# Kernel tuning notes

Measured on AMD Instinct MI355X. Metric: run time of the kernel, lower is better.

Reference implementation:

```python
import jax, jax.numpy as jnp
import numpy as np

B, T, S, A, H = 256, 256, 64, 16, 512  # batch, time, state_dim, action_dim, hypernet hidden


def setup_inputs() -> dict:
    key = jax.random.key(0)
    ks = jax.random.split(key, 12)
    x0 = jax.random.normal(ks[0], (B, S), dtype=jnp.float32)
    us = jax.random.normal(ks[1], (B, T, A), dtype=jnp.float32)
    # a_net: state_dim -> H -> S*S   (hypernetwork generating A(zx))
    Wa1 = jax.random.normal(ks[2], (S, H), dtype=jnp.float32) * 0.05
    ba1 = jax.random.normal(ks[3], (H,), dtype=jnp.float32) * 0.01
    Wa2 = jax.random.normal(ks[4], (H, S * S), dtype=jnp.float32) * 0.002  # small -> stable recurrence
    ba2 = jax.random.normal(ks[5], (S * S,), dtype=jnp.float32) * 0.002
    # b_net: action_dim -> H -> S*A  (hypernetwork generating B(zu))
    Wb1 = jax.random.normal(ks[6], (A, H), dtype=jnp.float32) * 0.05
    bb1 = jax.random.normal(ks[7], (H,), dtype=jnp.float32) * 0.01
    Wb2 = jax.random.normal(ks[8], (H, S * A), dtype=jnp.float32) * 0.02
    bb2 = jax.random.normal(ks[9], (S * A,), dtype=jnp.float32) * 0.02
    return {"x0": x0, "us": us, "Wa1": Wa1, "ba1": ba1, "Wa2": Wa2, "ba2": ba2,
            "Wb1": Wb1, "bb1": bb1, "Wb2": Wb2, "bb2": bb2}


def reference(x0, us, Wa1, ba1, Wa2, ba2, Wb1, bb1, Wb2, bb2):
    """HyperLinearSSM.rollout: x_{t+1} = A(x_t) @ x_t + B(u_t) @ u_t (zx=x, zu=u)."""
    def step(x, u):
        # hypernetwork-generated state matrix A(zx=x): [B, S, S]
        ha = jnp.tanh(x @ Wa1 + ba1)
        Amat = (ha @ Wa2 + ba2).reshape(-1, S, S)
        # hypernetwork-generated input matrix B(zu=u): [B, S, A]
        hb = jnp.tanh(u @ Wb1 + bb1)
        Bmat = (hb @ Wb2 + bb2).reshape(-1, S, A)
        x_next = jnp.einsum('bij,bj->bi', Amat, x) + jnp.einsum('bij,bj->bi', Bmat, u)
        return x_next, x_next

    us_t = jnp.transpose(us, (1, 0, 2))  # [T, B, A]
    _, xs = jax.lax.scan(step, x0, us_t)  # xs: [T, B, S]
    return jnp.transpose(xs, (1, 0, 2))   # [B, T, S]
```

## Files before the change

kernel.cpp:

```cpp
#include <hip/hip_runtime.h>

#define BSZ 256
#define TSZ 256
#define SSZ 64
#define ASZ 16
#define HSZ 512

typedef float f32x4 __attribute__((ext_vector_type(4)));
typedef short bf16x8 __attribute__((ext_vector_type(8)));
typedef unsigned short u16x8 __attribute__((ext_vector_type(8)));
typedef unsigned long long u64;
typedef unsigned short ushort_t;

#define XBUF_BYTES ((size_t)4 * BSZ * SSZ * sizeof(u64))
#define WT_ELEMS   ((size_t)4096 * 512)
#define WA1_ELEMS  ((size_t)64 * 512)
#define WS_NEEDED  (XBUF_BYTES + 3 * WT_ELEMS * sizeof(ushort_t) \
                    + 3 * WA1_ELEMS * sizeof(ushort_t))


#define XSTR        68
#define MF_X_OFF    0
#define MF_RED_OFF  4608
#define MF_HAH_OFF  5120
#define MF_HAM_OFF  (5120 + 18944)
#define MF_HAL_OFF  (24064 + 18944)
#define MF_WCH_OFF  (43008 + 18944)
#define MF_SMEM     (61952 + 2 * 49152)

#define NCH 16
#define HA_STR 20
#define X_OFF   0
#define HA_OFF  1024
#define W_OFF   (HA_OFF + HSZ * HA_STR)
#define RED_OFF (W_OFF + 3 * 32 * 256)
#define SMEM_FLOATS (RED_OFF + 512)
#define SMEM_BYTES  (SMEM_FLOATS * 4)

__device__ __forceinline__ void stage16(const void* gp, void* lp) {
    __builtin_amdgcn_global_load_lds(
        (const __attribute__((address_space(1))) void*)gp,
        (__attribute__((address_space(3))) void*)lp, 16, 0, 0);
}

__device__ __forceinline__ float wait_tag(const u64* p, unsigned tag) {
    u64 v = __hip_atomic_load(p, __ATOMIC_RELAXED, __HIP_MEMORY_SCOPE_AGENT);
    while ((unsigned)(v >> 32) != tag) {
        __builtin_amdgcn_s_sleep(1);
        v = __hip_atomic_load(p, __ATOMIC_RELAXED, __HIP_MEMORY_SCOPE_AGENT);
    }
    return __uint_as_float((unsigned)v);
}

__device__ __forceinline__ ushort_t f32_to_bf16(float f) {
    unsigned u = __float_as_uint(f);
    unsigned r = u + 0x7FFFu + ((u >> 16) & 1u);
    return (ushort_t)(r >> 16);
}
__device__ __forceinline__ float bf16_to_f32(ushort_t h) {
    return __uint_as_float((unsigned)h << 16);
}

__global__ __launch_bounds__(256) void wsplit_kernel(
    const float* __restrict__ Wa2,
    ushort_t* __restrict__ wth, ushort_t* __restrict__ wtm,
    ushort_t* __restrict__ wtl)
{
    __shared__ float tile[64][65];
    const int bc = blockIdx.x & 63;
    const int bh = blockIdx.x >> 6;
    const int c0 = bc * 64, h0 = bh * 64;
    const int tid = threadIdx.x;

    const int lr = tid >> 4, lc4 = (tid & 15) * 4;
    #pragma unroll
    for (int p = 0; p < 4; ++p) {
        const int h = p * 16 + lr;
        *(f32x4*)&tile[h][lc4] =
            *(const f32x4*)(Wa2 + (size_t)(h0 + h) * 4096 + c0 + lc4);
    }
    __syncthreads();

    const int col = tid >> 2, hb = (tid & 3) * 16;
    u16x8 H0, H1, M0, M1, L0, L1;
    #pragma unroll
    for (int q = 0; q < 16; ++q) {
        const float v = tile[hb + q][col];
        const ushort_t H = f32_to_bf16(v);
        const float r1 = v - bf16_to_f32(H);
        const ushort_t M = f32_to_bf16(r1);
        const ushort_t L = f32_to_bf16(r1 - bf16_to_f32(M));
        if (q < 8) { H0[q] = H; M0[q] = M; L0[q] = L; }
        else       { H1[q-8] = H; M1[q-8] = M; L1[q-8] = L; }
    }
    const int col_g = c0 + col;
    const int hbase = h0 + hb;
    const int kk    = hbase >> 5;
    const int sl0   = (hbase >> 3) & 3;
    const size_t atom0 = (((size_t)(col_g >> 5) * 16 + kk) * 4 + sl0) * 32
                       + (col_g & 31);
    const size_t atom1 = atom0 + 32;
    *(u16x8*)(wth + atom0 * 8) = H0;  *(u16x8*)(wth + atom1 * 8) = H1;
    *(u16x8*)(wtm + atom0 * 8) = M0;  *(u16x8*)(wtm + atom1 * 8) = M1;
    *(u16x8*)(wtl + atom0 * 8) = L0;  *(u16x8*)(wtl + atom1 * 8) = L1;
}

__global__ __launch_bounds__(256) void wsplit_wa1_kernel(
    const float* __restrict__ Wa1,
    ushort_t* __restrict__ wa1h, ushort_t* __restrict__ wa1m,
    ushort_t* __restrict__ wa1l)
{
    const int ht = blockIdx.x;
    const int t  = threadIdx.x;
    const int kk = t >> 7, slot = (t >> 5) & 3, col = t & 31;
    u16x8 H, M, L;
    #pragma unroll
    for (int e = 0; e < 8; ++e) {
        const int j = kk * 32 + slot * 8 + e;
        const float v = Wa1[(size_t)j * HSZ + ht * 32 + col];
        const ushort_t h16 = f32_to_bf16(v);
        const float r1 = v - bf16_to_f32(h16);
        const ushort_t m16 = f32_to_bf16(r1);
        const ushort_t l16 = f32_to_bf16(r1 - bf16_to_f32(m16));
        H[e] = h16; M[e] = m16; L[e] = l16;
    }
    const size_t off = (((size_t)(ht * 2 + kk) * 4 + slot) * 32 + col) * 8;
    *(u16x8*)(wa1h + off) = H;
    *(u16x8*)(wa1m + off) = M;
    *(u16x8*)(wa1l + off) = L;
}

__global__ __launch_bounds__(256) void bu_kernel(
    const float* __restrict__ us,
    const float* __restrict__ Wb1, const float* __restrict__ bb1,
    const float* __restrict__ Wb2, const float* __restrict__ bb2,
    float* __restrict__ out)
{
    __shared__ float u_lds[16][16];
    __shared__ float hb_lds[16][HSZ + 4];

    const int tid = threadIdx.x;
    const long s0 = (long)blockIdx.x * 16;

    u_lds[tid >> 4][tid & 15] = us[s0 * ASZ + tid];
    __syncthreads();

    #pragma unroll
    for (int rep = 0; rep < 2; ++rep) {
        const int h = tid + rep * 256;
        float acc[16];
        const float b1 = bb1[h];
        #pragma unroll
        for (int s = 0; s < 16; ++s) acc[s] = b1;
        #pragma unroll
        for (int a = 0; a < ASZ; ++a) {
            const float w = Wb1[a * HSZ + h];
            #pragma unroll
            for (int s = 0; s < 16; ++s) acc[s] += u_lds[s][a] * w;
        }
        #pragma unroll
        for (int s = 0; s < 16; ++s) hb_lds[s][h] = tanhf(acc[s]);
    }
    __syncthreads();

    const int i  = tid & 63;
    const int sg = tid >> 6;

    float ur[4][ASZ];
    #pragma unroll
    for (int s4 = 0; s4 < 4; ++s4)
        #pragma unroll
        for (int a = 0; a < ASZ; ++a) ur[s4][a] = u_lds[sg * 4 + s4][a];

    float acc[4];
    {
        float wb[ASZ];
        const float4* bp = (const float4*)(bb2 + i * ASZ);
        #pragma unroll
        for (int q = 0; q < 4; ++q) {
            float4 v = bp[q];
            wb[q*4+0] = v.x; wb[q*4+1] = v.y; wb[q*4+2] = v.z; wb[q*4+3] = v.w;
        }
        #pragma unroll
        for (int s4 = 0; s4 < 4; ++s4) {
            float t = 0.f;
            #pragma unroll
            for (int a = 0; a < ASZ; ++a) t += wb[a] * ur[s4][a];
            acc[s4] = t;
        }
    }

    for (int h = 0; h < HSZ; ++h) {
        float w[ASZ];
        const float4* wp = (const float4*)(Wb2 + (size_t)h * (SSZ * ASZ) + i * ASZ);
        #pragma unroll
        for (int q = 0; q < 4; ++q) {
            float4 v = wp[q];
            w[q*4+0] = v.x; w[q*4+1] = v.y; w[q*4+2] = v.z; w[q*4+3] = v.w;
        }
        #pragma unroll
        for (int s4 = 0; s4 < 4; ++s4) {
            float t = 0.f;
            #pragma unroll
            for (int a = 0; a < ASZ; ++a) t += w[a] * ur[s4][a];
            acc[s4] += hb_lds[sg * 4 + s4][h] * t;
        }
    }

    #pragma unroll
    for (int s4 = 0; s4 < 4; ++s4)
        out[(s0 + sg * 4 + s4) * SSZ + i] = acc[s4];
}

__global__ __launch_bounds__(512, 1) void ssm_mfma(
    const float* __restrict__ x0, const float* __restrict__ ba1,
    const ushort_t* __restrict__ wa1h, const ushort_t* __restrict__ wa1m,
    const ushort_t* __restrict__ wa1l,
    const ushort_t* __restrict__ wth, const ushort_t* __restrict__ wtm,
    const ushort_t* __restrict__ wtl, const float* __restrict__ ba2,
    float* __restrict__ out, u64* __restrict__ xbuf)
{
    extern __shared__ char smem[];
    float* x_lds = (float*)(smem + MF_X_OFF);
    float* red   = (float*)(smem + MF_RED_OFF);
    char*  haH   = smem + MF_HAH_OFF;
    char*  haM   = smem + MF_HAM_OFF;
    char*  haL   = smem + MF_HAL_OFF;
    char*  wch   = smem + MF_WCH_OFF;

    const int tid  = threadIdx.x;
    const int lane = tid & 63;
    const int wv   = tid >> 6;
    const int l15  = lane & 15, lg = lane >> 4;
    const int bt = blockIdx.x >> 4, ct = blockIdx.x & 15;
    const long bbase = (long)bt * 16;

    const size_t wtile = (size_t)((ct * 8 + wv) * 16) * 1024 + (size_t)lane * 8;

    const float ba2v0 = ba2[ct * 256 + 32 * wv + l15];
    const float ba2v1 = ba2[ct * 256 + 32 * wv + 16 + l15];
    const int jt  = 32 * (wv & 1) + l15;
    const int s_e = l15, q_e = lg;

    const int abyte  = lg * 288 + l15 * 16;
    const int b0byte = wv * 2048 + lg * 512 + l15 * 16;
    const int b1byte = b0byte + 256;

    float ba1r[4];
    #pragma unroll
    for (int cf = 0; cf < 4; ++cf) ba1r[cf] = ba1[wv * 64 + cf * 16 + l15];

    bf16x8 wf[4][6];
    #pragma unroll
    for (int cf = 0; cf < 4; ++cf) {
        const size_t o = (((size_t)(wv * 2 + (cf >> 1)) * 2 + 0) * 4 + lg) * 256
                       + ((cf & 1) * 16 + l15) * 8;
        wf[cf][0] = *(const bf16x8*)(wa1h + o);
        wf[cf][1] = *(const bf16x8*)(wa1m + o);
        wf[cf][2] = *(const bf16x8*)(wa1l + o);
        wf[cf][3] = *(const bf16x8*)(wa1h + o + 1024);
        wf[cf][4] = *(const bf16x8*)(wa1m + o + 1024);
        wf[cf][5] = *(const bf16x8*)(wa1l + o + 1024);
    }

    #define STAGEW(k_) do {                                                   \
        char* db_ = wch + ((k_) & 1) * 49152 + wv * 2048;                     \
        const ushort_t* gH_ = wth + wtile + (size_t)(k_) * 1024;              \
        const ushort_t* gM_ = wtm + wtile + (size_t)(k_) * 1024;              \
        const ushort_t* gL_ = wtl + wtile + (size_t)(k_) * 1024;              \
        stage16(gH_, db_);           stage16(gH_ + 512, db_ + 1024);          \
        stage16(gM_, db_ + 16384);   stage16(gM_ + 512, db_ + 16384 + 1024);  \
        stage16(gL_, db_ + 32768);   stage16(gL_ + 512, db_ + 32768 + 1024);  \
    } while (0)

    for (int t = 0; t < TSZ; ++t) {
        STAGEW(0);

        float bu_v = 0.f;
        if (wv == 0)
            bu_v = out[((bbase + s_e) * TSZ + t) * SSZ + (ct * 4 + q_e)];

        if (tid < 256) {
            const int sx = tid >> 4, jx = (tid & 15) * 4;
            float xv0, xv1, xv2, xv3;
            if (t > 0) {
                const u64* xs = xbuf + (size_t)((t - 1) & 3) * (BSZ * SSZ)
                              + (bbase + sx) * SSZ + jx;
                xv0 = wait_tag(xs + 0, (unsigned)t);
                xv1 = wait_tag(xs + 1, (unsigned)t);
                xv2 = wait_tag(xs + 2, (unsigned)t);
                xv3 = wait_tag(xs + 3, (unsigned)t);
            } else {
                const f32x4 x4 = *(const f32x4*)(x0 + (bbase + sx) * SSZ + jx);
                xv0 = x4.x; xv1 = x4.y; xv2 = x4.z; xv3 = x4.w;
            }
            x_lds[sx * XSTR + jx + 0] = xv0;
            x_lds[sx * XSTR + jx + 1] = xv1;
            x_lds[sx * XSTR + jx + 2] = xv2;
            x_lds[sx * XSTR + jx + 3] = xv3;
        }
        __syncthreads();

        bf16x8 xH[2], xM[2], xL[2];
        #pragma unroll
        for (int kk = 0; kk < 2; ++kk) {
            const float* xp = x_lds + l15 * XSTR + kk * 32 + lg * 8;
            const f32x4 a = *(const f32x4*)xp;
            const f32x4 b = *(const f32x4*)(xp + 4);
            #pragma unroll
            for (int e = 0; e < 8; ++e) {
                const float v = (e < 4) ? a[e] : b[e - 4];
                const ushort_t H = f32_to_bf16(v);
                const float r1 = v - bf16_to_f32(H);
                const ushort_t M = f32_to_bf16(r1);
                const ushort_t L = f32_to_bf16(r1 - bf16_to_f32(M));
                xH[kk][e] = (short)H; xM[kk][e] = (short)M; xL[kk][e] = (short)L;
            }
        }

        #pragma unroll
        for (int cf = 0; cf < 4; ++cf) {
            f32x4 hacc = {0.f, 0.f, 0.f, 0.f};
            hacc = __builtin_amdgcn_mfma_f32_16x16x32_bf16(xL[0], wf[cf][0], hacc, 0, 0, 0);
            hacc = __builtin_amdgcn_mfma_f32_16x16x32_bf16(xM[0], wf[cf][1], hacc, 0, 0, 0);
            hacc = __builtin_amdgcn_mfma_f32_16x16x32_bf16(xH[0], wf[cf][2], hacc, 0, 0, 0);
            hacc = __builtin_amdgcn_mfma_f32_16x16x32_bf16(xM[0], wf[cf][0], hacc, 0, 0, 0);
            hacc = __builtin_amdgcn_mfma_f32_16x16x32_bf16(xH[0], wf[cf][1], hacc, 0, 0, 0);
            hacc = __builtin_amdgcn_mfma_f32_16x16x32_bf16(xH[0], wf[cf][0], hacc, 0, 0, 0);
            hacc = __builtin_amdgcn_mfma_f32_16x16x32_bf16(xL[1], wf[cf][3], hacc, 0, 0, 0);
            hacc = __builtin_amdgcn_mfma_f32_16x16x32_bf16(xM[1], wf[cf][4], hacc, 0, 0, 0);
            hacc = __builtin_amdgcn_mfma_f32_16x16x32_bf16(xH[1], wf[cf][5], hacc, 0, 0, 0);
            hacc = __builtin_amdgcn_mfma_f32_16x16x32_bf16(xM[1], wf[cf][3], hacc, 0, 0, 0);
            hacc = __builtin_amdgcn_mfma_f32_16x16x32_bf16(xH[1], wf[cf][4], hacc, 0, 0, 0);
            hacc = __builtin_amdgcn_mfma_f32_16x16x32_bf16(xH[1], wf[cf][3], hacc, 0, 0, 0);

            const int kkg = wv * 2 + (cf >> 1);
            const int slt = (cf & 1) * 2 + (l15 >> 3);
            const int hwb = kkg * 1184 + slt * 288 + (l15 & 7) * 2;
            #pragma unroll
            for (int r = 0; r < 4; ++r) {
                const float v = tanhf(hacc[r] + ba1r[cf]);
                const ushort_t H = f32_to_bf16(v);
                const float r1 = v - bf16_to_f32(H);
                const ushort_t M = f32_to_bf16(r1);
                const ushort_t L = f32_to_bf16(r1 - bf16_to_f32(M));
                const int ad = hwb + (lg * 4 + r) * 16;
                *(ushort_t*)(haH + ad) = H;
                *(ushort_t*)(haM + ad) = M;
                *(ushort_t*)(haL + ad) = L;
            }
        }
        __syncthreads();

        f32x4 acc0 = {0.f, 0.f, 0.f, 0.f};
        f32x4 acc1 = {0.f, 0.f, 0.f, 0.f};
        #pragma unroll
        for (int k = 0; k < 16; ++k) {
            if (k + 1 < 16) {
                STAGEW(k + 1);
                asm volatile("s_waitcnt vmcnt(6)" ::: "memory");
            } else {
                asm volatile("s_waitcnt vmcnt(0)" ::: "memory");
            }
            __builtin_amdgcn_sched_barrier(0);

            const char* wb = wch + (k & 1) * 49152;
            const bf16x8 aH  = *(const bf16x8*)(haH + k * 1184 + abyte);
            const bf16x8 aM  = *(const bf16x8*)(haM + k * 1184 + abyte);
            const bf16x8 aL  = *(const bf16x8*)(haL + k * 1184 + abyte);
            const bf16x8 b0H = *(const bf16x8*)(wb + b0byte);
            const bf16x8 b0M = *(const bf16x8*)(wb + 16384 + b0byte);
            const bf16x8 b0L = *(const bf16x8*)(wb + 32768 + b0byte);
            const bf16x8 b1H = *(const bf16x8*)(wb + b1byte);
            const bf16x8 b1M = *(const bf16x8*)(wb + 16384 + b1byte);
            const bf16x8 b1L = *(const bf16x8*)(wb + 32768 + b1byte);

            acc0 = __builtin_amdgcn_mfma_f32_16x16x32_bf16(aL, b0H, acc0, 0, 0, 0);
            acc0 = __builtin_amdgcn_mfma_f32_16x16x32_bf16(aM, b0M, acc0, 0, 0, 0);
            acc0 = __builtin_amdgcn_mfma_f32_16x16x32_bf16(aH, b0L, acc0, 0, 0, 0);
            acc0 = __builtin_amdgcn_mfma_f32_16x16x32_bf16(aM, b0H, acc0, 0, 0, 0);
            acc0 = __builtin_amdgcn_mfma_f32_16x16x32_bf16(aH, b0M, acc0, 0, 0, 0);
            acc0 = __builtin_amdgcn_mfma_f32_16x16x32_bf16(aH, b0H, acc0, 0, 0, 0);
            acc1 = __builtin_amdgcn_mfma_f32_16x16x32_bf16(aL, b1H, acc1, 0, 0, 0);
            acc1 = __builtin_amdgcn_mfma_f32_16x16x32_bf16(aM, b1M, acc1, 0, 0, 0);
            acc1 = __builtin_amdgcn_mfma_f32_16x16x32_bf16(aH, b1L, acc1, 0, 0, 0);
            acc1 = __builtin_amdgcn_mfma_f32_16x16x32_bf16(aM, b1H, acc1, 0, 0, 0);
            acc1 = __builtin_amdgcn_mfma_f32_16x16x32_bf16(aH, b1M, acc1, 0, 0, 0);
            acc1 = __builtin_amdgcn_mfma_f32_16x16x32_bf16(aH, b1H, acc1, 0, 0, 0);
        }

        float part[4];
        #pragma unroll
        for (int r = 0; r < 4; ++r) {
            const int s = lg * 4 + r;
            part[r] = (acc0[r] + ba2v0) * x_lds[s * XSTR + jt]
                    + (acc1[r] + ba2v1) * x_lds[s * XSTR + jt + 16];
            part[r] += __shfl_xor(part[r], 1);
            part[r] += __shfl_xor(part[r], 2);
            part[r] += __shfl_xor(part[r], 4);
            part[r] += __shfl_xor(part[r], 8);
        }
        if (l15 == 0) {
            #pragma unroll
            for (int r = 0; r < 4; ++r)
                red[wv * 16 + lg * 4 + r] = part[r];
        }
        __syncthreads();

        if (wv == 0) {
            const long b = bbase + s_e;
            const int  i = ct * 4 + q_e;
            const float xn = red[(2 * q_e) * 16 + s_e]
                           + red[(2 * q_e + 1) * 16 + s_e] + bu_v;
            out[(b * TSZ + t) * SSZ + i] = xn;
            const u64 w = ((u64)(unsigned)(t + 1) << 32)
                        | (u64)__float_as_uint(xn);
            __hip_atomic_store(xbuf + (size_t)(t & 3) * (BSZ * SSZ) + b * SSZ + i,
                               w, __ATOMIC_RELAXED, __HIP_MEMORY_SCOPE_AGENT);
        }
    }
    #undef STAGEW
}

__global__ __launch_bounds__(512, 1) void ssm_f32(
    const float* __restrict__ x0,
    const float* __restrict__ Wa1, const float* __restrict__ ba1,
    const float* __restrict__ Wa2, const float* __restrict__ ba2,
    float* __restrict__ out, u64* __restrict__ xbuf)
{
    extern __shared__ float smemf[];
    float* x_lds = smemf + X_OFF;
    float* ha_t  = smemf + HA_OFF;
    float* wchf  = smemf + W_OFF;
    float* redf  = smemf + RED_OFF;

    const int tid  = threadIdx.x;
    const int lane = tid & 63;
    const int wv   = tid >> 6;
    const int bt = blockIdx.x >> 4;
    const int ct = blockIdx.x & 15;
    const long bbase = (long)bt * 16;

    const int c0 = ct * 256 + lane * 4;
    const f32x4 ba2r = *(const f32x4*)(ba2 + c0);
    const int j0 = (lane & 15) * 4;
    const int s_e = lane & 15, il_e = lane >> 4;

    for (int t = 0; t < TSZ; ++t) {
        #pragma unroll
        for (int it = 0; it < 4; ++it)
            stage16(Wa2 + (size_t)(wv * 4 + it) * 4096 + c0,
                    wchf + (0 * 32 + wv * 4 + it) * 256);
        #pragma unroll
        for (int it = 0; it < 4; ++it)
            stage16(Wa2 + (size_t)(32 + wv * 4 + it) * 4096 + c0,
                    wchf + (1 * 32 + wv * 4 + it) * 256);

        float bu_v = 0.f;
        if (wv == 0)
            bu_v = out[((bbase + s_e) * TSZ + t) * SSZ + (ct * 4 + il_e)];

        if (tid < 256) {
            const int sx = tid >> 4, jx = (tid & 15) * 4;
            float xv0, xv1, xv2, xv3;
            if (t > 0) {
                const u64* xs = xbuf + (size_t)((t - 1) & 3) * (BSZ * SSZ)
                              + (bbase + sx) * SSZ + jx;
                xv0 = wait_tag(xs + 0, (unsigned)t);
                xv1 = wait_tag(xs + 1, (unsigned)t);
                xv2 = wait_tag(xs + 2, (unsigned)t);
                xv3 = wait_tag(xs + 3, (unsigned)t);
            } else {
                const f32x4 x4 = *(const f32x4*)(x0 + (bbase + sx) * SSZ + jx);
                xv0 = x4.x; xv1 = x4.y; xv2 = x4.z; xv3 = x4.w;
            }
            x_lds[sx * SSZ + jx + 0] = xv0;
            x_lds[sx * SSZ + jx + 1] = xv1;
            x_lds[sx * SSZ + jx + 2] = xv2;
            x_lds[sx * SSZ + jx + 3] = xv3;
        }
        __syncthreads();

        {
            const int h0 = tid;
            float ar[16];
            const float b0 = ba1[h0];
            #pragma unroll
            for (int s = 0; s < 16; ++s) ar[s] = b0;
            #pragma unroll 4
            for (int jb = 0; jb < 16; ++jb) {
                float w0[4];
                #pragma unroll
                for (int q = 0; q < 4; ++q)
                    w0[q] = Wa1[(jb * 4 + q) * HSZ + h0];
                #pragma unroll
                for (int s = 0; s < 16; ++s) {
                    const f32x4 xr = *(const f32x4*)&x_lds[s * SSZ + jb * 4];
                    ar[s] += xr.x*w0[0] + xr.y*w0[1] + xr.z*w0[2] + xr.w*w0[3];
                }
            }
            #pragma unroll
            for (int s = 0; s < 16; ++s) ar[s] = tanhf(ar[s]);
            #pragma unroll
            for (int q = 0; q < 4; ++q) {
                f32x4 v0;
                v0.x=ar[q*4+0]; v0.y=ar[q*4+1]; v0.z=ar[q*4+2]; v0.w=ar[q*4+3];
                *(f32x4*)&ha_t[h0 * HA_STR + q * 4] = v0;
            }
        }
        __syncthreads();

        f32x4 acc[16];
        {
            const f32x4 zero = {0.f, 0.f, 0.f, 0.f};
            const f32x4 ini = (wv == 0) ? ba2r : zero;
            #pragma unroll
            for (int s = 0; s < 16; ++s) acc[s] = ini;
        }
        for (int k = 0; k < NCH; ++k) {
            if (k + 2 < NCH) {
                #pragma unroll
                for (int it = 0; it < 4; ++it)
                    stage16(Wa2 + (size_t)((k + 2) * 32 + wv * 4 + it) * 4096 + c0,
                            wchf + (((k + 2) % 3) * 32 + wv * 4 + it) * 256);
                asm volatile("s_waitcnt vmcnt(8)" ::: "memory");
            } else if (k + 1 < NCH) {
                asm volatile("s_waitcnt vmcnt(4)" ::: "memory");
            } else {
                asm volatile("s_waitcnt vmcnt(0)" ::: "memory");
            }
            __builtin_amdgcn_sched_barrier(0);

            const float* wb = wchf + (k % 3) * 8192 + (wv * 4) * 256;
            const float* hb = ha_t + (size_t)(k * 32 + wv * 4) * HA_STR;
            #pragma unroll
            for (int rr = 0; rr < 4; ++rr) {
                const f32x4 w4 = *(const f32x4*)(wb + rr * 256 + lane * 4);
                const f32x4 h0 = *(const f32x4*)(hb + rr * HA_STR + 0);
                const f32x4 h1 = *(const f32x4*)(hb + rr * HA_STR + 4);
                const f32x4 h2 = *(const f32x4*)(hb + rr * HA_STR + 8);
                const f32x4 h3 = *(const f32x4*)(hb + rr * HA_STR + 12);
                acc[0]  += h0.x * w4; acc[1]  += h0.y * w4;
                acc[2]  += h0.z * w4; acc[3]  += h0.w * w4;
                acc[4]  += h1.x * w4; acc[5]  += h1.y * w4;
                acc[6]  += h1.z * w4; acc[7]  += h1.w * w4;
                acc[8]  += h2.x * w4; acc[9]  += h2.y * w4;
                acc[10] += h2.z * w4; acc[11] += h2.w * w4;
                acc[12] += h3.x * w4; acc[13] += h3.y * w4;
                acc[14] += h3.z * w4; acc[15] += h3.w * w4;
            }
        }

        float part[16];
        #pragma unroll
        for (int s = 0; s < 16; ++s) {
            const f32x4 xr = *(const f32x4*)&x_lds[s * SSZ + j0];
            part[s] = acc[s].x*xr.x + acc[s].y*xr.y + acc[s].z*xr.z + acc[s].w*xr.w;
        }
        #pragma unroll
        for (int s = 0; s < 16; ++s) {
            part[s] += __shfl_xor(part[s], 1);
            part[s] += __shfl_xor(part[s], 2);
            part[s] += __shfl_xor(part[s], 4);
            part[s] += __shfl_xor(part[s], 8);
        }
        if ((lane & 15) == 0) {
            const int il = lane >> 4;
            #pragma unroll
            for (int s = 0; s < 16; ++s)
                redf[(wv * 4 + il) * 16 + s] = part[s];
        }
        __syncthreads();

        if (wv == 0) {
            const long b = bbase + s_e;
            const int  i = ct * 4 + il_e;
            float r = 0.f;
            #pragma unroll
            for (int w8 = 0; w8 < 8; ++w8)
                r += redf[(w8 * 4 + il_e) * 16 + s_e];
            const float xn = r + bu_v;
            out[(b * TSZ + t) * SSZ + i] = xn;
            const u64 w = ((u64)(unsigned)(t + 1) << 32)
                        | (u64)__float_as_uint(xn);
            __hip_atomic_store(xbuf + (size_t)(t & 3) * (BSZ * SSZ) + b * SSZ + i,
                               w, __ATOMIC_RELAXED, __HIP_MEMORY_SCOPE_AGENT);
        }
    }
}

extern "C" void kernel_launch(void* const* d_in, const int* in_sizes, int n_in,
                              void* d_out, int out_size, void* d_ws, size_t ws_size,
                              hipStream_t stream) {
    const float* x0  = (const float*)d_in[0];
    const float* us  = (const float*)d_in[1];
    const float* Wa1 = (const float*)d_in[2];
    const float* ba1 = (const float*)d_in[3];
    const float* Wa2 = (const float*)d_in[4];
    const float* ba2 = (const float*)d_in[5];
    const float* Wb1 = (const float*)d_in[6];
    const float* bb1 = (const float*)d_in[7];
    const float* Wb2 = (const float*)d_in[8];
    const float* bb2 = (const float*)d_in[9];
    float* out = (float*)d_out;

    u64* xbuf = (u64*)d_ws;
    hipMemsetAsync(xbuf, 0, XBUF_BYTES, stream);

    hipLaunchKernelGGL(bu_kernel, dim3((BSZ * TSZ) / 16), dim3(256), 0, stream,
                       us, Wb1, bb1, Wb2, bb2, out);

    if (ws_size >= WS_NEEDED) {
        ushort_t* wth  = (ushort_t*)((char*)d_ws + XBUF_BYTES);
        ushort_t* wtm  = wth + WT_ELEMS;
        ushort_t* wtl  = wtm + WT_ELEMS;
        ushort_t* wa1h = wtl + WT_ELEMS;
        ushort_t* wa1m = wa1h + WA1_ELEMS;
        ushort_t* wa1l = wa1m + WA1_ELEMS;
        hipLaunchKernelGGL(wsplit_kernel, dim3(512), dim3(256), 0, stream,
                           Wa2, wth, wtm, wtl);
        hipLaunchKernelGGL(wsplit_wa1_kernel, dim3(16), dim3(256), 0, stream,
                           Wa1, wa1h, wa1m, wa1l);
        (void)hipFuncSetAttribute((const void*)ssm_mfma,
                                  hipFuncAttributeMaxDynamicSharedMemorySize, MF_SMEM);
        void* args[] = {(void*)&x0, (void*)&ba1,
                        (void*)&wa1h, (void*)&wa1m, (void*)&wa1l,
                        (void*)&wth, (void*)&wtm, (void*)&wtl, (void*)&ba2,
                        (void*)&out, (void*)&xbuf};
        hipLaunchCooperativeKernel((const void*)ssm_mfma, dim3(256), dim3(512),
                                   args, MF_SMEM, stream);
    } else {
        (void)hipFuncSetAttribute((const void*)ssm_f32,
                                  hipFuncAttributeMaxDynamicSharedMemorySize, SMEM_BYTES);
        void* args[] = {(void*)&x0, (void*)&Wa1, (void*)&ba1,
                        (void*)&Wa2, (void*)&ba2, (void*)&out, (void*)&xbuf};
        hipLaunchCooperativeKernel((const void*)ssm_f32, dim3(256), dim3(512),
                                   args, SMEM_BYTES, stream);
    }
}
```

Before: 8.318 ms.

## Add per-batch-tile arrival counter and reload Wa1 fragments instead of holding in registers

Adds a per-(batch tile, timestep) atomic counter that each of the 16 column blocks increments after publishing its slice of x. Before reading x, one thread spins on the counter with s_sleep, replacing many threads each polling tagged xbuf entries. The Wa1 bf16 fragments are also now loaded from global memory every step instead of being kept in registers, which lowers register pressure but adds global/L2 traffic on the critical path. The tag check is kept, so there is now a two-stage wait.

```diff
diff --git a/kernel.cpp b/kernel.cpp
--- a/kernel.cpp
+++ b/kernel.cpp
@@ -13,9 +13,10 @@
 typedef unsigned short ushort_t;
 
 #define XBUF_BYTES ((size_t)4 * BSZ * SSZ * sizeof(u64))
+#define CNT_BYTES  ((size_t)16 * TSZ * sizeof(unsigned))
 #define WT_ELEMS   ((size_t)4096 * 512)
 #define WA1_ELEMS  ((size_t)64 * 512)
-#define WS_NEEDED  (XBUF_BYTES + 3 * WT_ELEMS * sizeof(ushort_t) \
+#define WS_NEEDED  (XBUF_BYTES + CNT_BYTES + 3 * WT_ELEMS * sizeof(ushort_t) \
                     + 3 * WA1_ELEMS * sizeof(ushort_t))
 
 
@@ -218,7 +219,8 @@
     const ushort_t* __restrict__ wa1l,
     const ushort_t* __restrict__ wth, const ushort_t* __restrict__ wtm,
     const ushort_t* __restrict__ wtl, const float* __restrict__ ba2,
-    float* __restrict__ out, u64* __restrict__ xbuf)
+    float* __restrict__ out, u64* __restrict__ xbuf,
+    unsigned* __restrict__ cnt)
 {
     extern __shared__ char smem[];
     float* x_lds = (float*)(smem + MF_X_OFF);
@@ -250,18 +252,13 @@
     #pragma unroll
     for (int cf = 0; cf < 4; ++cf) ba1r[cf] = ba1[wv * 64 + cf * 16 + l15];
 
-    bf16x8 wf[4][6];
-    #pragma unroll
-    for (int cf = 0; cf < 4; ++cf) {
-        const size_t o = (((size_t)(wv * 2 + (cf >> 1)) * 2 + 0) * 4 + lg) * 256
-                       + ((cf & 1) * 16 + l15) * 8;
-        wf[cf][0] = *(const bf16x8*)(wa1h + o);
-        wf[cf][1] = *(const bf16x8*)(wa1m + o);
-        wf[cf][2] = *(const bf16x8*)(wa1l + o);
-        wf[cf][3] = *(const bf16x8*)(wa1h + o + 1024);
-        wf[cf][4] = *(const bf16x8*)(wa1m + o + 1024);
-        wf[cf][5] = *(const bf16x8*)(wa1l + o + 1024);
-    }
+    size_t wa1o[4];
+    #pragma unroll
+    for (int cf = 0; cf < 4; ++cf)
+        wa1o[cf] = (((size_t)(wv * 2 + (cf >> 1)) * 2 + 0) * 4 + lg) * 256
+                 + ((cf & 1) * 16 + l15) * 8;
+
+    unsigned* mycnt = cnt + bt * TSZ;
 
     #define STAGEW(k_) do {                                                   \
         char* db_ = wch + ((k_) & 1) * 49152 + wv * 2048;                     \
@@ -279,6 +276,15 @@
         float bu_v = 0.f;
         if (wv == 0)
             bu_v = out[((bbase + s_e) * TSZ + t) * SSZ + (ct * 4 + q_e)];
+
+        if (t > 0) {
+            if (tid == 0) {
+                while (__hip_atomic_load(&mycnt[t - 1], __ATOMIC_RELAXED,
+                                         __HIP_MEMORY_SCOPE_AGENT) < 16u)
+                    __builtin_amdgcn_s_sleep(2);
+            }
+            __syncthreads();
+        }
 
         if (tid < 256) {
             const int sx = tid >> 4, jx = (tid & 15) * 4;
@@ -320,19 +326,25 @@
 
         #pragma unroll
         for (int cf = 0; cf < 4; ++cf) {
+            const bf16x8 wH0 = *(const bf16x8*)(wa1h + wa1o[cf]);
+            const bf16x8 wM0 = *(const bf16x8*)(wa1m + wa1o[cf]);
+            const bf16x8 wL0 = *(const bf16x8*)(wa1l + wa1o[cf]);
+            const bf16x8 wH1 = *(const bf16x8*)(wa1h + wa1o[cf] + 1024);
+            const bf16x8 wM1 = *(const bf16x8*)(wa1m + wa1o[cf] + 1024);
+            const bf16x8 wL1 = *(const bf16x8*)(wa1l + wa1o[cf] + 1024);
             f32x4 hacc = {0.f, 0.f, 0.f, 0.f};
-            hacc = __builtin_amdgcn_mfma_f32_16x16x32_bf16(xL[0], wf[cf][0], hacc, 0, 0, 0);
-            hacc = __builtin_amdgcn_mfma_f32_16x16x32_bf16(xM[0], wf[cf][1], hacc, 0, 0, 0);
-            hacc = __builtin_amdgcn_mfma_f32_16x16x32_bf16(xH[0], wf[cf][2], hacc, 0, 0, 0);
-            hacc = __builtin_amdgcn_mfma_f32_16x16x32_bf16(xM[0], wf[cf][0], hacc, 0, 0, 0);
-            hacc = __builtin_amdgcn_mfma_f32_16x16x32_bf16(xH[0], wf[cf][1], hacc, 0, 0, 0);
-            hacc = __builtin_amdgcn_mfma_f32_16x16x32_bf16(xH[0], wf[cf][0], hacc, 0, 0, 0);
-            hacc = __builtin_amdgcn_mfma_f32_16x16x32_bf16(xL[1], wf[cf][3], hacc, 0, 0, 0);
-            hacc = __builtin_amdgcn_mfma_f32_16x16x32_bf16(xM[1], wf[cf][4], hacc, 0, 0, 0);
-            hacc = __builtin_amdgcn_mfma_f32_16x16x32_bf16(xH[1], wf[cf][5], hacc, 0, 0, 0);
-            hacc = __builtin_amdgcn_mfma_f32_16x16x32_bf16(xM[1], wf[cf][3], hacc, 0, 0, 0);
-            hacc = __builtin_amdgcn_mfma_f32_16x16x32_bf16(xH[1], wf[cf][4], hacc, 0, 0, 0);
-            hacc = __builtin_amdgcn_mfma_f32_16x16x32_bf16(xH[1], wf[cf][3], hacc, 0, 0, 0);
+            hacc = __builtin_amdgcn_mfma_f32_16x16x32_bf16(xL[0], wH0, hacc, 0, 0, 0);
+            hacc = __builtin_amdgcn_mfma_f32_16x16x32_bf16(xM[0], wM0, hacc, 0, 0, 0);
+            hacc = __builtin_amdgcn_mfma_f32_16x16x32_bf16(xH[0], wL0, hacc, 0, 0, 0);
+            hacc = __builtin_amdgcn_mfma_f32_16x16x32_bf16(xM[0], wH0, hacc, 0, 0, 0);
+            hacc = __builtin_amdgcn_mfma_f32_16x16x32_bf16(xH[0], wM0, hacc, 0, 0, 0);
+            hacc = __builtin_amdgcn_mfma_f32_16x16x32_bf16(xH[0], wH0, hacc, 0, 0, 0);
+            hacc = __builtin_amdgcn_mfma_f32_16x16x32_bf16(xL[1], wH1, hacc, 0, 0, 0);
+            hacc = __builtin_amdgcn_mfma_f32_16x16x32_bf16(xM[1], wM1, hacc, 0, 0, 0);
+            hacc = __builtin_amdgcn_mfma_f32_16x16x32_bf16(xH[1], wL1, hacc, 0, 0, 0);
+            hacc = __builtin_amdgcn_mfma_f32_16x16x32_bf16(xM[1], wH1, hacc, 0, 0, 0);
+            hacc = __builtin_amdgcn_mfma_f32_16x16x32_bf16(xH[1], wM1, hacc, 0, 0, 0);
+            hacc = __builtin_amdgcn_mfma_f32_16x16x32_bf16(xH[1], wH1, hacc, 0, 0, 0);
 
             const int kkg = wv * 2 + (cf >> 1);
             const int slt = (cf & 1) * 2 + (l15 >> 3);
@@ -417,6 +429,10 @@
                         | (u64)__float_as_uint(xn);
             __hip_atomic_store(xbuf + (size_t)(t & 3) * (BSZ * SSZ) + b * SSZ + i,
                                w, __ATOMIC_RELAXED, __HIP_MEMORY_SCOPE_AGENT);
+            asm volatile("s_waitcnt vmcnt(0)" ::: "memory");
+            if (lane == 0)
+                __hip_atomic_fetch_add(&mycnt[t], 1u, __ATOMIC_RELAXED,
+                                       __HIP_MEMORY_SCOPE_AGENT);
         }
     }
     #undef STAGEW
@@ -605,13 +621,14 @@
     float* out = (float*)d_out;
 
     u64* xbuf = (u64*)d_ws;
-    hipMemsetAsync(xbuf, 0, XBUF_BYTES, stream);
+    unsigned* cnt = (unsigned*)((char*)d_ws + XBUF_BYTES);
+    hipMemsetAsync(d_ws, 0, XBUF_BYTES + CNT_BYTES, stream);
 
     hipLaunchKernelGGL(bu_kernel, dim3((BSZ * TSZ) / 16), dim3(256), 0, stream,
                        us, Wb1, bb1, Wb2, bb2, out);
 
     if (ws_size >= WS_NEEDED) {
-        ushort_t* wth  = (ushort_t*)((char*)d_ws + XBUF_BYTES);
+        ushort_t* wth  = (ushort_t*)((char*)d_ws + XBUF_BYTES + CNT_BYTES);
         ushort_t* wtm  = wth + WT_ELEMS;
         ushort_t* wtl  = wtm + WT_ELEMS;
         ushort_t* wa1h = wtl + WT_ELEMS;
@@ -626,7 +643,7 @@
         void* args[] = {(void*)&x0, (void*)&ba1,
                         (void*)&wa1h, (void*)&wa1m, (void*)&wa1l,
                         (void*)&wth, (void*)&wtm, (void*)&wtl, (void*)&ba2,
-                        (void*)&out, (void*)&xbuf};
+                        (void*)&out, (void*)&xbuf, (void*)&cnt};
         hipLaunchCooperativeKernel((const void*)ssm_mfma, dim3(256), dim3(512),
                                    args, MF_SMEM, stream);
     } else {
```

Measured after the change: 8.741 ms. 1.05x slower.
